# Kernel tuning notes

Measured on AMD Instinct MI355X. Metric: run time of the kernel, lower is better.

## Reference

```python
import jax, jax.numpy as jnp
import numpy as np

B, S, D, H, PF = 2, 2048, 1024, 16, 4096
HD = D // H
EPS = 1e-5


def _rope_tables(seq_len, dim, theta=10000.0):
    freqs = 1.0 / (theta ** (np.arange(0, dim, 2)[: dim // 2].astype(np.float32) / dim))
    ang = np.outer(np.arange(seq_len, dtype=np.float32), freqs)  # [S, D/2]
    return jnp.asarray(np.cos(ang)), jnp.asarray(np.sin(ang))


def setup_inputs() -> dict:
    key = jax.random.key(0)
    ks = jax.random.split(key, 16)
    s = 0.02
    inp = {
        "src": jax.random.normal(ks[0], (B, S, D), dtype=jnp.float32),
        "Wq": jax.random.normal(ks[1], (D, D), dtype=jnp.float32) * s,
        "bq": jnp.zeros((D,), jnp.float32),
        "Wk": jax.random.normal(ks[2], (D, D), dtype=jnp.float32) * s,
        "bk": jnp.zeros((D,), jnp.float32),
        "Wv": jax.random.normal(ks[3], (D, D), dtype=jnp.float32) * s,
        "bv": jnp.zeros((D,), jnp.float32),
        "Wo": jax.random.normal(ks[4], (D, D), dtype=jnp.float32) * s,
        "bo": jnp.zeros((D,), jnp.float32),
        "ln1_g": jnp.ones((D,), jnp.float32),
        "ln1_b": jnp.zeros((D,), jnp.float32),
        "W1": jax.random.normal(ks[5], (D, PF), dtype=jnp.float32) * s,
        "b1": jnp.zeros((PF,), jnp.float32),
        "W2": jax.random.normal(ks[6], (PF, D), dtype=jnp.float32) * s,
        "b2": jnp.zeros((D,), jnp.float32),
        "ln2_g": jnp.ones((D,), jnp.float32),
        "ln2_b": jnp.zeros((D,), jnp.float32),
    }
    cos, sin = _rope_tables(S, D)
    inp["rope_cos"] = cos
    inp["rope_sin"] = sin
    return inp


def _apply_rope(x, cos, sin):
    # x: [B, S, D]; rotate adjacent channel pairs as complex numbers (Meta LLaMA style)
    xp = x.reshape(x.shape[0], x.shape[1], -1, 2)
    a, b = xp[..., 0], xp[..., 1]
    c = cos[None, : x.shape[1]]
    s = sin[None, : x.shape[1]]
    out = jnp.stack([a * c - b * s, a * s + b * c], axis=-1)
    return out.reshape(x.shape)


def _layer_norm(x, g, b):
    mu = x.mean(-1, keepdims=True)
    var = ((x - mu) ** 2).mean(-1, keepdims=True)
    return (x - mu) * jax.lax.rsqrt(var + EPS) * g + b


def reference(src, Wq, bq, Wk, bk, Wv, bv, Wo, bo, ln1_g, ln1_b,
              W1, b1, W2, b2, ln2_g, ln2_b, rope_cos, rope_sin):
    bsz, seq, _ = src.shape
    Q = src @ Wq + bq
    K = src @ Wk + bk
    V = src @ Wv + bv
    Q = _apply_rope(Q, rope_cos, rope_sin)
    K = _apply_rope(K, rope_cos, rope_sin)
    # split heads: [B, H, S, HD]
    Q = Q.reshape(bsz, seq, H, HD).transpose(0, 2, 1, 3)
    K = K.reshape(bsz, seq, H, HD).transpose(0, 2, 1, 3)
    V = V.reshape(bsz, seq, H, HD).transpose(0, 2, 1, 3)
    scale = 1.0 / jnp.sqrt(jnp.float32(HD))
    energy = jnp.einsum("bhqd,bhkd->bhqk", Q, K) * scale
    attn = jax.nn.softmax(energy, axis=-1)
    x = jnp.einsum("bhqk,bhkd->bhqd", attn, V)
    x = x.transpose(0, 2, 1, 3).reshape(bsz, seq, D)
    attn_out = x @ Wo + bo
    # residual + LayerNorm
    h = _layer_norm(src + attn_out, ln1_g, ln1_b)
    # positionwise feedforward
    ff = jax.nn.relu(h @ W1 + b1) @ W2 + b2
    return _layer_norm(h + ff, ln2_g, ln2_b)
```

## Files before the change

### kernel.cpp

```cpp
#include <hip/hip_runtime.h>

#define SEQ 2048
#define DIM 1024
#define NH 16
#define HDIM 64
#define PFF 4096
#define NROWS 4096
#define BATCH 2
#define NQKV 3072

typedef unsigned short u16;
typedef unsigned int u32;
typedef __attribute__((ext_vector_type(8))) short short8;
typedef __attribute__((ext_vector_type(4))) float f32x4;
typedef __attribute__((ext_vector_type(16))) float f32x16;

__device__ inline float b2f(u16 u){ return __uint_as_float(((u32)u)<<16); }
__device__ inline u16 f2b(float f){
  u32 u = __float_as_uint(f);
  u32 r = u + 0x7FFFu + ((u>>16)&1u);
  return (u16)(r>>16);
}
__device__ __forceinline__ float fexp2(float x){
  float r; asm("v_exp_f32 %0, %1" : "=v"(r) : "v"(x)); return r;
}
__device__ __forceinline__ float fmax3(float a, float b, float c){
  float r; asm("v_max3_f32 %0, %1, %2, %3" : "=v"(r) : "v"(a), "v"(b), "v"(c)); return r;
}

#define AS1C(p) ((const __attribute__((address_space(1))) unsigned int*)(p))
#define AS3P(p) ((__attribute__((address_space(3))) unsigned int*)(p))

__global__ void k_cast_bf16(const float* __restrict__ in, u16* __restrict__ out, int n4){
  int i = blockIdx.x*256 + threadIdx.x;
  if (i >= n4) return;
  float4 v = ((const float4*)in)[i];
  ushort4 o;
  o.x = f2b(v.x); o.y = f2b(v.y); o.z = f2b(v.z); o.w = f2b(v.w);
  ((ushort4*)out)[i] = o;
}

__global__ __launch_bounds__(256) void k_transpose_cast(const float* __restrict__ in,
                                                        u16* __restrict__ out, int R, int C){
  __shared__ float tile[32][33];
  int tx = threadIdx.x & 31, ty = threadIdx.x >> 5;
  int c0 = blockIdx.x*32, r0 = blockIdx.y*32;
  #pragma unroll
  for (int i=0;i<4;++i)
    tile[ty+i*8][tx] = in[(size_t)(r0+ty+i*8)*C + c0 + tx];
  __syncthreads();
  #pragma unroll
  for (int i=0;i<4;++i)
    out[(size_t)(c0+ty+i*8)*R + r0 + tx] = f2b(tile[tx][ty+i*8]);
}

__global__ __launch_bounds__(256) void k_transpose_v(const u16* __restrict__ QKV, u16* __restrict__ VT){
  __shared__ u16 tile[32][34];
  int tx = threadIdx.x & 31, ty = threadIdx.x >> 5;
  int d0 = blockIdx.x*32, r0 = blockIdx.y*32;
  #pragma unroll
  for (int i=0;i<4;++i)
    tile[ty+i*8][tx] = QKV[(size_t)(r0+ty+i*8)*NQKV + 2048 + d0 + tx];
  __syncthreads();
  #pragma unroll
  for (int i=0;i<4;++i)
    VT[(size_t)(d0+ty+i*8)*NROWS + r0 + tx] = tile[tx][ty+i*8];
}

__global__ void k_pack3(const float* __restrict__ a, const float* __restrict__ b,
                        const float* __restrict__ c, float* __restrict__ o){
  int i = blockIdx.x*256 + threadIdx.x;
  if (i >= NQKV) return;
  o[i] = i < 1024 ? a[i] : (i < 2048 ? b[i-1024] : c[i-2048]);
}

template<bool RELU, bool BF16OUT, int SPLIT>
__global__ __launch_bounds__(512, 2) void k_gemm256(
    const u16* __restrict__ A, const u16* __restrict__ Bt,
    const float* __restrict__ bias, void* __restrict__ Cp,
    int M, int N, int Kc, int lda, int ldb){
  extern __shared__ char lds[];
  const int tid = threadIdx.x;
  const int lane = tid & 63, wid = tid >> 6;
  const int quad = lane >> 4, l15 = lane & 15;
  const int wm = wid >> 2, wn = wid & 3;
  const int ro = (l15*4 + quad)*16;
  const int srow = lane >> 2;
  const int sk   = (lane & 3)*8;
  const int nwg = gridDim.x * gridDim.y;
  int lid = blockIdx.y * gridDim.x + blockIdx.x;
  lid = (lid & 7) * (nwg >> 3) + (lid >> 3);
  const int bx = lid % gridDim.x, by = lid / gridDim.x;
  const int rowBase = by*256, colBase = bx*256;
  const u16* Az = A  + (size_t)blockIdx.z * Kc;
  const u16* Bz = Bt + (size_t)blockIdx.z * Kc;

  f32x4 acc[8][4] = {};

  auto stage2 = [&](int buf, int k0, int i){
    int idx = i*8 + wid;
    int rs = idx >> 1, ks = idx & 1;
    const u16* ga = Az + (size_t)(rowBase + rs*16 + srow)*lda + k0 + ks*32 + sk;
    __builtin_amdgcn_global_load_lds(AS1C(ga), AS3P(lds + buf*65536 + idx*1024), 16, 0, 0);
    const u16* gb = Bz + (size_t)(colBase + rs*16 + srow)*ldb + k0 + ks*32 + sk;
    __builtin_amdgcn_global_load_lds(AS1C(gb), AS3P(lds + buf*65536 + 32768 + idx*1024), 16, 0, 0);
  };

  #pragma unroll
  for (int i=0;i<4;++i) stage2(0, 0, i);
  __syncthreads();

  const int NT = Kc >> 6;
  #pragma unroll 1
  for (int t=0; t<NT; ++t){
    const int buf = t & 1;
    const bool pf = (t+1 < NT);
    const int k0n = (t+1)*64;
    char* Ab = lds + buf*65536;
    char* Bb = Ab + 32768;
    short8 a0[4][2], a1[4][2], b0[2][2], b1[2][2];

    #pragma unroll
    for (int mf=0; mf<4; ++mf)
      #pragma unroll
      for (int kk=0; kk<2; ++kk)
        a0[mf][kk] = *(const short8*)(Ab + ((wm*8+mf)*2+kk)*1024 + ro);
    #pragma unroll
    for (int nf=0; nf<2; ++nf)
      #pragma unroll
      for (int kk=0; kk<2; ++kk)
        b0[nf][kk] = *(const short8*)(Bb + ((wn*4+nf)*2+kk)*1024 + ro);
    if (pf){ stage2(buf^1, k0n, 0); stage2(buf^1, k0n, 1); }
    __builtin_amdgcn_s_barrier();
    __builtin_amdgcn_s_setprio(1);
    #pragma unroll
    for (int mf=0; mf<4; ++mf)
      #pragma unroll
      for (int nf=0; nf<2; ++nf)
        #pragma unroll
        for (int kk=0; kk<2; ++kk)
          acc[mf][nf] = __builtin_amdgcn_mfma_f32_16x16x32_bf16(a0[mf][kk], b0[nf][kk], acc[mf][nf], 0,0,0);
    __builtin_amdgcn_s_setprio(0);
    __builtin_amdgcn_s_barrier();

    #pragma unroll
    for (int nf=0; nf<2; ++nf)
      #pragma unroll
      for (int kk=0; kk<2; ++kk)
        b1[nf][kk] = *(const short8*)(Bb + ((wn*4+2+nf)*2+kk)*1024 + ro);
    if (pf){ stage2(buf^1, k0n, 2); stage2(buf^1, k0n, 3); }
    __builtin_amdgcn_s_barrier();
    __builtin_amdgcn_s_setprio(1);
    #pragma unroll
    for (int mf=0; mf<4; ++mf)
      #pragma unroll
      for (int nf=0; nf<2; ++nf)
        #pragma unroll
        for (int kk=0; kk<2; ++kk)
          acc[mf][2+nf] = __builtin_amdgcn_mfma_f32_16x16x32_bf16(a0[mf][kk], b1[nf][kk], acc[mf][2+nf], 0,0,0);
    __builtin_amdgcn_s_setprio(0);
    __builtin_amdgcn_s_barrier();

    #pragma unroll
    for (int mf=0; mf<4; ++mf)
      #pragma unroll
      for (int kk=0; kk<2; ++kk)
        a1[mf][kk] = *(const short8*)(Ab + ((wm*8+4+mf)*2+kk)*1024 + ro);
    __builtin_amdgcn_s_barrier();
    __builtin_amdgcn_s_setprio(1);
    #pragma unroll
    for (int mf=0; mf<4; ++mf)
      #pragma unroll
      for (int nf=0; nf<2; ++nf)
        #pragma unroll
        for (int kk=0; kk<2; ++kk)
          acc[4+mf][2+nf] = __builtin_amdgcn_mfma_f32_16x16x32_bf16(a1[mf][kk], b1[nf][kk], acc[4+mf][2+nf], 0,0,0);
    __builtin_amdgcn_s_setprio(0);
    __builtin_amdgcn_s_barrier();

    if (pf) asm volatile("s_waitcnt vmcnt(0)" ::: "memory");
    __builtin_amdgcn_s_barrier();
    __builtin_amdgcn_s_setprio(1);
    #pragma unroll
    for (int mf=0; mf<4; ++mf)
      #pragma unroll
      for (int nf=0; nf<2; ++nf)
        #pragma unroll
        for (int kk=0; kk<2; ++kk)
          acc[4+mf][nf] = __builtin_amdgcn_mfma_f32_16x16x32_bf16(a1[mf][kk], b0[nf][kk], acc[4+mf][nf], 0,0,0);
    __builtin_amdgcn_s_setprio(0);
    __builtin_amdgcn_s_barrier();
  }

  u16* Cb = (u16*)Cp + (SPLIT > 1 ? (size_t)blockIdx.z * M * N : 0);
  float* Cf = (float*)Cp + (SPLIT > 1 ? (size_t)blockIdx.z * M * N : 0);
  #pragma unroll
  for (int mf=0; mf<8; ++mf){
    #pragma unroll
    for (int nf=0; nf<4; ++nf){
      int col = colBase + wn*64 + nf*16 + l15;
      float bv = (SPLIT == 1 || blockIdx.z == 0) ? bias[col] : 0.f;
      #pragma unroll
      for (int j=0; j<4; ++j){
        int row = rowBase + wm*128 + mf*16 + quad*4 + j;
        float v = acc[mf][nf][j] + bv;
        if (RELU) v = fmaxf(v, 0.f);
        if (BF16OUT) Cb[(size_t)row*N + col] = f2b(v);
        else         Cf[(size_t)row*N + col] = v;
      }
    }
  }
}

template<bool RELU, bool BF16OUT, bool BIAS>
__global__ __launch_bounds__(256) void k_gemm(
    const u16* __restrict__ A, const u16* __restrict__ Bt,
    const float* __restrict__ bias, void* __restrict__ Cp,
    int M, int N, int Kc, int lda, int ldb){
  __shared__ __align__(16) char lds[32768];
  const int tid = threadIdx.x;
  const int lane = tid & 63, wid = tid >> 6;
  const int quad = lane >> 4, l15 = lane & 15;
  const int wr = wid >> 1, wc = wid & 1;
  const int nwg = gridDim.x * gridDim.y;
  int lid = blockIdx.y * gridDim.x + blockIdx.x;
  lid = (lid & 7) * (nwg >> 3) + (lid >> 3);
  const int bx = lid % gridDim.x, by = lid / gridDim.x;
  const int rowBase = by * 128, colBase = bx * 128;
  const u16* Az = A  + (size_t)blockIdx.z * Kc;
  const u16* Bz = Bt + (size_t)blockIdx.z * Kc;
  f32x4 acc[4][4] = {};
  const int srow = lane >> 3;
  const int scol = lane & 7;
  for (int k0 = 0; k0 < Kc; k0 += 64) {
    __syncthreads();
    #pragma unroll
    for (int i=0;i<4;++i){
      int wch = wid*4 + i;
      int row = wch*8 + srow;
      int c   = scol ^ (row & 7);
      const u16* ga = Az + (size_t)(rowBase+row)*lda + k0 + c*8;
      __builtin_amdgcn_global_load_lds(AS1C(ga), AS3P(lds + wch*1024), 16, 0, 0);
      const u16* gb = Bz + (size_t)(colBase+row)*ldb + k0 + c*8;
      __builtin_amdgcn_global_load_lds(AS1C(gb), AS3P(lds + 16384 + wch*1024), 16, 0, 0);
    }
    __syncthreads();
    #pragma unroll
    for (int kk=0;kk<2;++kk){
      short8 af[4], bfr[4];
      #pragma unroll
      for (int m=0;m<4;++m){
        int r = wr*64 + m*16 + l15;
        af[m] = *(const short8*)(lds + ((r*128 + kk*64 + quad*16) ^ ((r&7)<<4)));
      }
      #pragma unroll
      for (int n=0;n<4;++n){
        int r = wc*64 + n*16 + l15;
        bfr[n] = *(const short8*)(lds + 16384 + ((r*128 + kk*64 + quad*16) ^ ((r&7)<<4)));
      }
      __builtin_amdgcn_s_setprio(1);
      #pragma unroll
      for (int m=0;m<4;++m)
        #pragma unroll
        for (int n=0;n<4;++n)
          acc[m][n] = __builtin_amdgcn_mfma_f32_16x16x32_bf16(af[m], bfr[n], acc[m][n], 0,0,0);
      __builtin_amdgcn_s_setprio(0);
    }
  }
  float* Cf = (float*)Cp + (size_t)blockIdx.z * M * N;
  #pragma unroll
  for (int m=0;m<4;++m){
    #pragma unroll
    for (int n=0;n<4;++n){
      int col = colBase + wc*64 + n*16 + l15;
      float bv = (BIAS && blockIdx.z == 0) ? bias[col] : 0.f;
      #pragma unroll
      for (int j=0;j<4;++j){
        int row = rowBase + wr*64 + m*16 + quad*4 + j;
        float v = acc[m][n][j] + bv;
        if (RELU) v = fmaxf(v, 0.f);
        if (BF16OUT) ((u16*)Cp)[(size_t)row*N + col] = f2b(v);
        else         Cf[(size_t)row*N + col] = v;
      }
    }
  }
}

__global__ void k_rope(u16* __restrict__ QKV,
                       const float* __restrict__ cosT, const float* __restrict__ sinT){
  int idx = blockIdx.x*256 + threadIdx.x;
  int row = idx >> 9, p = idx & 511;
  int s = row & (SEQ-1);
  float c = cosT[s*512 + p], sn = sinT[s*512 + p];
  u16* qp = QKV + (size_t)row*NQKV + 2*p;
  u16* kp = qp + 1024;
  ushort2 q = *(ushort2*)qp;
  ushort2 k = *(ushort2*)kp;
  float qx = b2f(q.x), qy = b2f(q.y), kx = b2f(k.x), ky = b2f(k.y);
  const float scale = 0.125f * 1.44269504f;
  ushort2 qo, ko;
  qo.x = f2b((qx*c - qy*sn)*scale);
  qo.y = f2b((qx*sn + qy*c)*scale);
  ko.x = f2b(kx*c - ky*sn);
  ko.y = f2b(kx*sn + ky*c);
  *(ushort2*)qp = qo;
  *(ushort2*)kp = ko;
}

__global__ __launch_bounds__(256) void k_attn(
    const u16* __restrict__ QKV, const u16* __restrict__ VT, u16* __restrict__ Xo){
  const int qt = blockIdx.x, h = blockIdx.y, b = blockIdx.z;
  const int tid = threadIdx.x, lane = tid & 63, wid = tid >> 6;
  const int l31 = lane & 31, hi = lane >> 5;
  __shared__ __align__(16) char lds[32768];
  const int srow = lane >> 3, scol = lane & 7;

  short8 qf[4];
  {
    const u16* qrow = QKV + (size_t)(b*SEQ + qt*128 + wid*32 + l31)*NQKV + h*HDIM;
    #pragma unroll
    for (int dk=0; dk<4; ++dk)
      qf[dk] = *(const short8*)(qrow + dk*16 + 8*hi);
  }
  float m_run = -1e30f, s_run = 0.f;
  f32x16 oacc[2] = {};
  const size_t krow0 = (size_t)(b*SEQ);

  auto do_stage = [&](int buf, int kt){
    char* kdst = lds + buf*16384;
    char* vdst = kdst + 8192;
    #pragma unroll
    for (int i=0;i<2;++i){
      int wch = wid*2 + i;
      int row = wch*8 + srow;
      int c = scol ^ (row & 7);
      const u16* gk = QKV + (krow0 + kt*64 + row)*NQKV + 1024 + h*HDIM + c*8;
      __builtin_amdgcn_global_load_lds(AS1C(gk), AS3P(kdst + wch*1024), 16, 0, 0);
      const u16* gv = VT + (size_t)(h*HDIM + row)*NROWS + b*SEQ + kt*64 + c*8;
      __builtin_amdgcn_global_load_lds(AS1C(gv), AS3P(vdst + wch*1024), 16, 0, 0);
    }
  };

  auto do_tile = [&](int buf){
    char* kb = lds + buf*16384;
    char* vb = kb + 8192;
    f32x16 pacc[2] = {};
    __builtin_amdgcn_s_setprio(1);
    #pragma unroll
    for (int kbk=0;kbk<2;++kbk){
      #pragma unroll
      for (int dk=0;dk<4;++dk){
        int row = kbk*32 + l31;
        short8 kf = *(const short8*)(kb + ((row*128 + dk*32 + 16*hi) ^ ((row&7)<<4)));
        pacc[kbk] = __builtin_amdgcn_mfma_f32_32x32x16_bf16(kf, qf[dk], pacc[kbk], 0,0,0);
      }
    }
    __builtin_amdgcn_s_setprio(0);
    float tmax = fmaxf(pacc[0][0], pacc[0][1]);
    #pragma unroll
    for (int r=2;r<16;r+=2) tmax = fmax3(tmax, pacc[0][r], pacc[0][r+1]);
    #pragma unroll
    for (int r=0;r<16;r+=2) tmax = fmax3(tmax, pacc[1][r], pacc[1][r+1]);
    tmax = fmaxf(tmax, __shfl_xor(tmax, 32));
    if (__any(tmax > m_run + 8.0f)){
      float mnew = fmaxf(m_run, tmax);
      float a = fexp2(m_run - mnew);
      s_run *= a;
      m_run = mnew;
      #pragma unroll
      for (int r=0;r<16;++r){
        int src = (r&3) + 8*(r>>2) + 4*hi;
        float ar = __shfl(a, src);
        oacc[0][r] *= ar;
        oacc[1][r] *= ar;
      }
    }
    float p[2][16];
    float psum = 0.f;
    #pragma unroll
    for (int kbk=0;kbk<2;++kbk)
      #pragma unroll
      for (int r=0;r<16;++r){
        float e = fexp2(pacc[kbk][r] - m_run);
        p[kbk][r] = e;
        psum += e;
      }
    psum += __shfl_xor(psum, 32);
    s_run += psum;
    short8 pa[4];
    #pragma unroll
    for (int kbk=0;kbk<2;++kbk){
      #pragma unroll
      for (int s=0;s<2;++s){
        u32 X0, X1, Y0, Y1;
        asm("v_cvt_pk_bf16_f32 %0, %1, %2" : "=v"(X0) : "v"(p[kbk][8*s+0]), "v"(p[kbk][8*s+1]));
        asm("v_cvt_pk_bf16_f32 %0, %1, %2" : "=v"(X1) : "v"(p[kbk][8*s+2]), "v"(p[kbk][8*s+3]));
        asm("v_cvt_pk_bf16_f32 %0, %1, %2" : "=v"(Y0) : "v"(p[kbk][8*s+4]), "v"(p[kbk][8*s+5]));
        asm("v_cvt_pk_bf16_f32 %0, %1, %2" : "=v"(Y1) : "v"(p[kbk][8*s+6]), "v"(p[kbk][8*s+7]));
        asm volatile("v_permlane32_swap_b32 %0, %1" : "+v"(X0), "+v"(Y0));
        asm volatile("v_permlane32_swap_b32 %0, %1" : "+v"(X1), "+v"(Y1));
        union { u32 w[4]; short8 s8; } pu;
        pu.w[0] = X0; pu.w[1] = X1; pu.w[2] = Y0; pu.w[3] = Y1;
        pa[2*kbk+s] = pu.s8;
      }
    }
    __builtin_amdgcn_s_setprio(1);
    #pragma unroll
    for (int db=0;db<2;++db){
      #pragma unroll
      for (int ks=0;ks<4;++ks){
        int row = db*32 + l31;
        short8 vf = *(const short8*)(vb + ((row*128 + ks*32 + 16*hi) ^ ((row&7)<<4)));
        oacc[db] = __builtin_amdgcn_mfma_f32_32x32x16_bf16(pa[ks], vf, oacc[db], 0,0,0);
      }
    }
    __builtin_amdgcn_s_setprio(0);
  };

  do_stage(0, 0);
  __syncthreads();
  const int NT = SEQ/64;
  #pragma unroll 1
  for (int kt=0; kt<NT; kt+=2){
    do_stage(1, kt+1);
    do_tile(0);
    __syncthreads();
    if (kt+2 < NT) do_stage(0, kt+2);
    do_tile(1);
    __syncthreads();
  }
  #pragma unroll
  for (int r=0;r<16;++r){
    int crow = (r&3) + 8*(r>>2) + 4*hi;
    float sq = __shfl(s_run, crow);
    float rs = __builtin_amdgcn_rcpf(sq);
    int grow = b*SEQ + qt*128 + wid*32 + crow;
    Xo[(size_t)grow*DIM + h*HDIM + l31]      = f2b(oacc[0][r] * rs);
    Xo[(size_t)grow*DIM + h*HDIM + 32 + l31] = f2b(oacc[1][r] * rs);
  }
}

template<int PARTS, bool WBF>
__global__ __launch_bounds__(256) void k_ln(
    const float* __restrict__ a, const float* __restrict__ p0, const float* __restrict__ p1,
    const float* __restrict__ g, const float* __restrict__ be,
    float* __restrict__ outf, u16* __restrict__ outb){
  const int row = blockIdx.x, tid = threadIdx.x;
  __shared__ float red[8];
  float4 av = ((const float4*)(a  + (size_t)row*DIM))[tid];
  float4 b0 = ((const float4*)(p0 + (size_t)row*DIM))[tid];
  float4 b1 = ((const float4*)(p1 + (size_t)row*DIM))[tid];
  float x0 = av.x+b0.x+b1.x, x1 = av.y+b0.y+b1.y, x2 = av.z+b0.z+b1.z, x3 = av.w+b0.w+b1.w;
  float s = x0+x1+x2+x3;
  #pragma unroll
  for (int o=32;o>=1;o>>=1) s += __shfl_down(s, o);
  if ((tid&63)==0) red[tid>>6] = s;
  __syncthreads();
  float mean = (red[0]+red[1]+red[2]+red[3]) * (1.0f/DIM);
  float d0=x0-mean, d1=x1-mean, d2=x2-mean, d3=x3-mean;
  float vs = d0*d0+d1*d1+d2*d2+d3*d3;
  #pragma unroll
  for (int o=32;o>=1;o>>=1) vs += __shfl_down(vs, o);
  if ((tid&63)==0) red[4+(tid>>6)] = vs;
  __syncthreads();
  float var = (red[4]+red[5]+red[6]+red[7]) * (1.0f/DIM);
  float rs = rsqrtf(var + 1e-5f);
  float4 gv = ((const float4*)g)[tid];
  float4 bev = ((const float4*)be)[tid];
  float4 y;
  y.x = d0*rs*gv.x + bev.x;
  y.y = d1*rs*gv.y + bev.y;
  y.z = d2*rs*gv.z + bev.z;
  y.w = d3*rs*gv.w + bev.w;
  ((float4*)(outf + (size_t)row*DIM))[tid] = y;
  if (WBF){
    ushort4 o4; o4.x=f2b(y.x); o4.y=f2b(y.y); o4.z=f2b(y.z); o4.w=f2b(y.w);
    ((ushort4*)(outb + (size_t)row*DIM))[tid] = o4;
  }
}

template<int PARTS>
__global__ __launch_bounds__(256) void k_lnp(
    const float* __restrict__ a, const u16* __restrict__ p,
    const float* __restrict__ g, const float* __restrict__ be,
    float* __restrict__ outf){
  const int row = blockIdx.x, tid = threadIdx.x;
  __shared__ float red[8];
  float4 av = ((const float4*)(a + (size_t)row*DIM))[tid];
  float x0 = av.x, x1 = av.y, x2 = av.z, x3 = av.w;
  #pragma unroll
  for (int z=0; z<PARTS; ++z){
    ushort4 pv = ((const ushort4*)(p + (size_t)z*NROWS*DIM + (size_t)row*DIM))[tid];
    x0 += b2f(pv.x); x1 += b2f(pv.y); x2 += b2f(pv.z); x3 += b2f(pv.w);
  }
  float s = x0+x1+x2+x3;
  #pragma unroll
  for (int o=32;o>=1;o>>=1) s += __shfl_down(s, o);
  if ((tid&63)==0) red[tid>>6] = s;
  __syncthreads();
  float mean = (red[0]+red[1]+red[2]+red[3]) * (1.0f/DIM);
  float d0=x0-mean, d1=x1-mean, d2=x2-mean, d3=x3-mean;
  float vs = d0*d0+d1*d1+d2*d2+d3*d3;
  #pragma unroll
  for (int o=32;o>=1;o>>=1) vs += __shfl_down(vs, o);
  if ((tid&63)==0) red[4+(tid>>6)] = vs;
  __syncthreads();
  float var = (red[4]+red[5]+red[6]+red[7]) * (1.0f/DIM);
  float rs = rsqrtf(var + 1e-5f);
  float4 gv = ((const float4*)g)[tid];
  float4 bev = ((const float4*)be)[tid];
  float4 y;
  y.x = d0*rs*gv.x + bev.x;
  y.y = d1*rs*gv.y + bev.y;
  y.z = d2*rs*gv.z + bev.z;
  y.w = d3*rs*gv.w + bev.w;
  ((float4*)(outf + (size_t)row*DIM))[tid] = y;
}

extern "C" void kernel_launch(void* const* d_in, const int* in_sizes, int n_in,
                              void* d_out, int out_size, void* d_ws, size_t ws_size,
                              hipStream_t stream){
  (void)in_sizes; (void)n_in; (void)out_size; (void)ws_size;
  const float* src  = (const float*)d_in[0];
  const float* Wq   = (const float*)d_in[1];
  const float* bq   = (const float*)d_in[2];
  const float* Wk   = (const float*)d_in[3];
  const float* bk   = (const float*)d_in[4];
  const float* Wv   = (const float*)d_in[5];
  const float* bv   = (const float*)d_in[6];
  const float* Wo   = (const float*)d_in[7];
  const float* bo   = (const float*)d_in[8];
  const float* ln1g = (const float*)d_in[9];
  const float* ln1b = (const float*)d_in[10];
  const float* W1   = (const float*)d_in[11];
  const float* b1   = (const float*)d_in[12];
  const float* W2   = (const float*)d_in[13];
  const float* b2   = (const float*)d_in[14];
  const float* ln2g = (const float*)d_in[15];
  const float* ln2b = (const float*)d_in[16];
  const float* rc   = (const float*)d_in[17];
  const float* rsn  = (const float*)d_in[18];

  char* ws = (char*)d_ws;
  const size_t MB = (size_t)1<<20;
  u16* Xbf   = (u16*)(ws);
  u16* QKV   = (u16*)(ws + 8*MB);
  u16* VTb   = (u16*)(ws + 32*MB);
  float* aop   = (float*)(ws + 8*MB);
  u16* ff2b  = (u16*)(ws + 8*MB);
  u16* xat   = (u16*)(ws + 40*MB);
  u16* hbf   = (u16*)(ws + 48*MB);
  u16* WqkvT = (u16*)(ws + 56*MB);
  u16* WoT   = (u16*)(ws + 62*MB);
  u16* W1T   = (u16*)(ws + 64*MB);
  u16* W2T   = (u16*)(ws + 72*MB);
  u16* ff1   = (u16*)(ws + 80*MB);
  float* h   = (float*)(ws + 112*MB);
  float* bqkv= (float*)(ws + 128*MB);
  const size_t P16 = 16*MB/4;

  hipFuncSetAttribute((const void*)&k_gemm256<false,true,1>,
                      hipFuncAttributeMaxDynamicSharedMemorySize, 131072);
  hipFuncSetAttribute((const void*)&k_gemm256<true,true,1>,
                      hipFuncAttributeMaxDynamicSharedMemorySize, 131072);
  hipFuncSetAttribute((const void*)&k_gemm256<false,true,4>,
                      hipFuncAttributeMaxDynamicSharedMemorySize, 131072);

  dim3 blk(256);
  k_cast_bf16<<<dim3(NROWS*DIM/1024), blk, 0, stream>>>(src, Xbf, NROWS*DIM/4);
  k_transpose_cast<<<dim3(DIM/32, DIM/32), blk, 0, stream>>>(Wq, WqkvT, DIM, DIM);
  k_transpose_cast<<<dim3(DIM/32, DIM/32), blk, 0, stream>>>(Wk, WqkvT + (size_t)1024*1024, DIM, DIM);
  k_transpose_cast<<<dim3(DIM/32, DIM/32), blk, 0, stream>>>(Wv, WqkvT + (size_t)2048*1024, DIM, DIM);
  k_transpose_cast<<<dim3(DIM/32, DIM/32), blk, 0, stream>>>(Wo, WoT, DIM, DIM);
  k_transpose_cast<<<dim3(PFF/32, DIM/32), blk, 0, stream>>>(W1, W1T, DIM, PFF);
  k_transpose_cast<<<dim3(DIM/32, PFF/32), blk, 0, stream>>>(W2, W2T, PFF, DIM);
  k_pack3<<<dim3(12), blk, 0, stream>>>(bq, bk, bv, bqkv);

  k_gemm256<false,true,1><<<dim3(NQKV/256, NROWS/256), dim3(512), 131072, stream>>>(
      Xbf, WqkvT, bqkv, QKV, NROWS, NQKV, DIM, DIM, DIM);
  k_rope<<<dim3(NROWS*512/256), blk, 0, stream>>>(QKV, rc, rsn);
  k_transpose_v<<<dim3(DIM/32, NROWS/32), blk, 0, stream>>>(QKV, VTb);
  k_attn<<<dim3(SEQ/128, NH, BATCH), blk, 0, stream>>>(QKV, VTb, xat);
  k_gemm<false,false,true><<<dim3(DIM/128, NROWS/128, 2), blk, 0, stream>>>(
      xat, WoT, bo, aop, NROWS, DIM, 512, DIM, DIM);
  k_ln<2,true><<<dim3(NROWS), blk, 0, stream>>>(src, aop, aop + P16, ln1g, ln1b, h, hbf);
  k_gemm256<true,true,1><<<dim3(PFF/256, NROWS/256), dim3(512), 131072, stream>>>(
      hbf, W1T, b1, ff1, NROWS, PFF, DIM, DIM, DIM);
  k_gemm256<false,true,4><<<dim3(DIM/256, NROWS/256, 4), dim3(512), 131072, stream>>>(
      ff1, W2T, b2, ff2b, NROWS, DIM, 1024, PFF, PFF);
  k_lnp<4><<<dim3(NROWS), blk, 0, stream>>>(h, ff2b, ln2g, ln2b, (float*)d_out);
}
```

Before: 250.8 us.

## Triple-buffer attention KV tiles and overlap QK with softmax-PV; bf16 out-proj partials

Result: no change. 254.9 us (+1.6%).

```diff
diff --git a/kernel.cpp b/kernel.cpp
--- a/kernel.cpp
+++ b/kernel.cpp
@@ -267,6 +267,7 @@
       __builtin_amdgcn_s_setprio(0);
     }
   }
+  u16* Cb = (u16*)Cp + (size_t)blockIdx.z * M * N;
   float* Cf = (float*)Cp + (size_t)blockIdx.z * M * N;
   #pragma unroll
   for (int m=0;m<4;++m){
@@ -279,7 +280,7 @@
         int row = rowBase + wr*64 + m*16 + quad*4 + j;
         float v = acc[m][n][j] + bv;
         if (RELU) v = fmaxf(v, 0.f);
-        if (BF16OUT) ((u16*)Cp)[(size_t)row*N + col] = f2b(v);
+        if (BF16OUT) Cb[(size_t)row*N + col] = f2b(v);
         else         Cf[(size_t)row*N + col] = v;
       }
     }
@@ -312,7 +313,7 @@
   const int qt = blockIdx.x, h = blockIdx.y, b = blockIdx.z;
   const int tid = threadIdx.x, lane = tid & 63, wid = tid >> 6;
   const int l31 = lane & 31, hi = lane >> 5;
-  __shared__ __align__(16) char lds[32768];
+  __shared__ __align__(16) char lds[49152];
   const int srow = lane >> 3, scol = lane & 7;
 
   short8 qf[4];
@@ -326,8 +327,8 @@
   f32x16 oacc[2] = {};
   const size_t krow0 = (size_t)(b*SEQ);
 
-  auto do_stage = [&](int buf, int kt){
-    char* kdst = lds + buf*16384;
+  auto stage = [&](int kt){
+    char* kdst = lds + (kt%3)*16384;
     char* vdst = kdst + 8192;
     #pragma unroll
     for (int i=0;i<2;++i){
@@ -341,10 +342,10 @@
     }
   };
 
-  auto do_tile = [&](int buf){
-    char* kb = lds + buf*16384;
-    char* vb = kb + 8192;
-    f32x16 pacc[2] = {};
+  auto qk = [&](int kt, f32x16 (&pacc)[2]){
+    char* kb = lds + (kt%3)*16384;
+    #pragma unroll
+    for (int r=0;r<16;++r){ pacc[0][r]=0.f; pacc[1][r]=0.f; }
     __builtin_amdgcn_s_setprio(1);
     #pragma unroll
     for (int kbk=0;kbk<2;++kbk){
@@ -356,6 +357,10 @@
       }
     }
     __builtin_amdgcn_s_setprio(0);
+  };
+
+  auto sm_pv = [&](int kt, f32x16 (&pacc)[2]){
+    char* vb = lds + (kt%3)*16384 + 8192;
     float tmax = fmaxf(pacc[0][0], pacc[0][1]);
     #pragma unroll
     for (int r=2;r<16;r+=2) tmax = fmax3(tmax, pacc[0][r], pacc[0][r+1]);
@@ -375,28 +380,26 @@
         oacc[1][r] *= ar;
       }
     }
-    float p[2][16];
     float psum = 0.f;
-    #pragma unroll
-    for (int kbk=0;kbk<2;++kbk)
-      #pragma unroll
-      for (int r=0;r<16;++r){
-        float e = fexp2(pacc[kbk][r] - m_run);
-        p[kbk][r] = e;
-        psum += e;
-      }
-    psum += __shfl_xor(psum, 32);
-    s_run += psum;
     short8 pa[4];
     #pragma unroll
     for (int kbk=0;kbk<2;++kbk){
       #pragma unroll
       for (int s=0;s<2;++s){
+        float e0 = fexp2(pacc[kbk][8*s+0] - m_run);
+        float e1 = fexp2(pacc[kbk][8*s+1] - m_run);
+        float e2 = fexp2(pacc[kbk][8*s+2] - m_run);
+        float e3 = fexp2(pacc[kbk][8*s+3] - m_run);
+        float e4 = fexp2(pacc[kbk][8*s+4] - m_run);
+        float e5 = fexp2(pacc[kbk][8*s+5] - m_run);
+        float e6 = fexp2(pacc[kbk][8*s+6] - m_run);
+        float e7 = fexp2(pacc[kbk][8*s+7] - m_run);
+        psum += (e0+e1)+(e2+e3)+((e4+e5)+(e6+e7));
         u32 X0, X1, Y0, Y1;
-        asm("v_cvt_pk_bf16_f32 %0, %1, %2" : "=v"(X0) : "v"(p[kbk][8*s+0]), "v"(p[kbk][8*s+1]));
-        asm("v_cvt_pk_bf16_f32 %0, %1, %2" : "=v"(X1) : "v"(p[kbk][8*s+2]), "v"(p[kbk][8*s+3]));
-        asm("v_cvt_pk_bf16_f32 %0, %1, %2" : "=v"(Y0) : "v"(p[kbk][8*s+4]), "v"(p[kbk][8*s+5]));
-        asm("v_cvt_pk_bf16_f32 %0, %1, %2" : "=v"(Y1) : "v"(p[kbk][8*s+6]), "v"(p[kbk][8*s+7]));
+        asm("v_cvt_pk_bf16_f32 %0, %1, %2" : "=v"(X0) : "v"(e0), "v"(e1));
+        asm("v_cvt_pk_bf16_f32 %0, %1, %2" : "=v"(X1) : "v"(e2), "v"(e3));
+        asm("v_cvt_pk_bf16_f32 %0, %1, %2" : "=v"(Y0) : "v"(e4), "v"(e5));
+        asm("v_cvt_pk_bf16_f32 %0, %1, %2" : "=v"(Y1) : "v"(e6), "v"(e7));
         asm volatile("v_permlane32_swap_b32 %0, %1" : "+v"(X0), "+v"(Y0));
         asm volatile("v_permlane32_swap_b32 %0, %1" : "+v"(X1), "+v"(Y1));
         union { u32 w[4]; short8 s8; } pu;
@@ -404,6 +407,8 @@
         pa[2*kbk+s] = pu.s8;
       }
     }
+    psum += __shfl_xor(psum, 32);
+    s_run += psum;
     __builtin_amdgcn_s_setprio(1);
     #pragma unroll
     for (int db=0;db<2;++db){
@@ -417,17 +422,35 @@
     __builtin_amdgcn_s_setprio(0);
   };
 
-  do_stage(0, 0);
-  __syncthreads();
+  f32x16 paccA[2], paccB[2];
   const int NT = SEQ/64;
+  stage(0);
+  stage(1);
+  asm volatile("s_waitcnt vmcnt(4)" ::: "memory");
+  __builtin_amdgcn_s_barrier();
+  qk(0, paccA);
   #pragma unroll 1
-  for (int kt=0; kt<NT; kt+=2){
-    do_stage(1, kt+1);
-    do_tile(0);
-    __syncthreads();
-    if (kt+2 < NT) do_stage(0, kt+2);
-    do_tile(1);
-    __syncthreads();
+  for (int t=0; t<NT; t+=2){
+    if (t+2 < NT){
+      stage(t+2);
+      asm volatile("s_waitcnt vmcnt(4)" ::: "memory");
+    } else {
+      asm volatile("s_waitcnt vmcnt(0)" ::: "memory");
+    }
+    __builtin_amdgcn_s_barrier();
+    qk(t+1, paccB);
+    sm_pv(t, paccA);
+    __builtin_amdgcn_s_barrier();
+    if (t+3 < NT){
+      stage(t+3);
+      asm volatile("s_waitcnt vmcnt(4)" ::: "memory");
+    } else {
+      asm volatile("s_waitcnt vmcnt(0)" ::: "memory");
+    }
+    __builtin_amdgcn_s_barrier();
+    if (t+2 < NT) qk(t+2, paccA);
+    sm_pv(t+1, paccB);
+    __builtin_amdgcn_s_barrier();
   }
   #pragma unroll
   for (int r=0;r<16;++r){
@@ -441,16 +464,19 @@
 }
 
 template<int PARTS, bool WBF>
-__global__ __launch_bounds__(256) void k_ln(
-    const float* __restrict__ a, const float* __restrict__ p0, const float* __restrict__ p1,
+__global__ __launch_bounds__(256) void k_lnp(
+    const float* __restrict__ a, const u16* __restrict__ p,
     const float* __restrict__ g, const float* __restrict__ be,
     float* __restrict__ outf, u16* __restrict__ outb){
   const int row = blockIdx.x, tid = threadIdx.x;
   __shared__ float red[8];
-  float4 av = ((const float4*)(a  + (size_t)row*DIM))[tid];
-  float4 b0 = ((const float4*)(p0 + (size_t)row*DIM))[tid];
-  float4 b1 = ((const float4*)(p1 + (size_t)row*DIM))[tid];
-  float x0 = av.x+b0.x+b1.x, x1 = av.y+b0.y+b1.y, x2 = av.z+b0.z+b1.z, x3 = av.w+b0.w+b1.w;
+  float4 av = ((const float4*)(a + (size_t)row*DIM))[tid];
+  float x0 = av.x, x1 = av.y, x2 = av.z, x3 = av.w;
+  #pragma unroll
+  for (int z=0; z<PARTS; ++z){
+    ushort4 pv = ((const ushort4*)(p + (size_t)z*NROWS*DIM + (size_t)row*DIM))[tid];
+    x0 += b2f(pv.x); x1 += b2f(pv.y); x2 += b2f(pv.z); x3 += b2f(pv.w);
+  }
   float s = x0+x1+x2+x3;
   #pragma unroll
   for (int o=32;o>=1;o>>=1) s += __shfl_down(s, o);
@@ -477,44 +503,6 @@
     ushort4 o4; o4.x=f2b(y.x); o4.y=f2b(y.y); o4.z=f2b(y.z); o4.w=f2b(y.w);
     ((ushort4*)(outb + (size_t)row*DIM))[tid] = o4;
   }
-}
-
-template<int PARTS>
-__global__ __launch_bounds__(256) void k_lnp(
-    const float* __restrict__ a, const u16* __restrict__ p,
-    const float* __restrict__ g, const float* __restrict__ be,
-    float* __restrict__ outf){
-  const int row = blockIdx.x, tid = threadIdx.x;
-  __shared__ float red[8];
-  float4 av = ((const float4*)(a + (size_t)row*DIM))[tid];
-  float x0 = av.x, x1 = av.y, x2 = av.z, x3 = av.w;
-  #pragma unroll
-  for (int z=0; z<PARTS; ++z){
-    ushort4 pv = ((const ushort4*)(p + (size_t)z*NROWS*DIM + (size_t)row*DIM))[tid];
-    x0 += b2f(pv.x); x1 += b2f(pv.y); x2 += b2f(pv.z); x3 += b2f(pv.w);
-  }
-  float s = x0+x1+x2+x3;
-  #pragma unroll
-  for (int o=32;o>=1;o>>=1) s += __shfl_down(s, o);
-  if ((tid&63)==0) red[tid>>6] = s;
-  __syncthreads();
-  float mean = (red[0]+red[1]+red[2]+red[3]) * (1.0f/DIM);
-  float d0=x0-mean, d1=x1-mean, d2=x2-mean, d3=x3-mean;
-  float vs = d0*d0+d1*d1+d2*d2+d3*d3;
-  #pragma unroll
-  for (int o=32;o>=1;o>>=1) vs += __shfl_down(vs, o);
-  if ((tid&63)==0) red[4+(tid>>6)] = vs;
-  __syncthreads();
-  float var = (red[4]+red[5]+red[6]+red[7]) * (1.0f/DIM);
-  float rs = rsqrtf(var + 1e-5f);
-  float4 gv = ((const float4*)g)[tid];
-  float4 bev = ((const float4*)be)[tid];
-  float4 y;
-  y.x = d0*rs*gv.x + bev.x;
-  y.y = d1*rs*gv.y + bev.y;
-  y.z = d2*rs*gv.z + bev.z;
-  y.w = d3*rs*gv.w + bev.w;
-  ((float4*)(outf + (size_t)row*DIM))[tid] = y;
 }
 
 extern "C" void kernel_launch(void* const* d_in, const int* in_sizes, int n_in,
@@ -546,7 +534,7 @@
   u16* Xbf   = (u16*)(ws);
   u16* QKV   = (u16*)(ws + 8*MB);
   u16* VTb   = (u16*)(ws + 32*MB);
-  float* aop   = (float*)(ws + 8*MB);
+  u16* aob   = (u16*)(ws + 8*MB);
   u16* ff2b  = (u16*)(ws + 8*MB);
   u16* xat   = (u16*)(ws + 40*MB);
   u16* hbf   = (u16*)(ws + 48*MB);
@@ -557,7 +545,6 @@
   u16* ff1   = (u16*)(ws + 80*MB);
   float* h   = (float*)(ws + 112*MB);
   float* bqkv= (float*)(ws + 128*MB);
-  const size_t P16 = 16*MB/4;
 
   hipFuncSetAttribute((const void*)&k_gemm256<false,true,1>,
                       hipFuncAttributeMaxDynamicSharedMemorySize, 131072);
@@ -581,12 +568,12 @@
   k_rope<<<dim3(NROWS*512/256), blk, 0, stream>>>(QKV, rc, rsn);
   k_transpose_v<<<dim3(DIM/32, NROWS/32), blk, 0, stream>>>(QKV, VTb);
   k_attn<<<dim3(SEQ/128, NH, BATCH), blk, 0, stream>>>(QKV, VTb, xat);
-  k_gemm<false,false,true><<<dim3(DIM/128, NROWS/128, 2), blk, 0, stream>>>(
-      xat, WoT, bo, aop, NROWS, DIM, 512, DIM, DIM);
-  k_ln<2,true><<<dim3(NROWS), blk, 0, stream>>>(src, aop, aop + P16, ln1g, ln1b, h, hbf);
+  k_gemm<false,true,true><<<dim3(DIM/128, NROWS/128, 2), blk, 0, stream>>>(
+      xat, WoT, bo, aob, NROWS, DIM, 512, DIM, DIM);
+  k_lnp<2,true><<<dim3(NROWS), blk, 0, stream>>>(src, aob, ln1g, ln1b, h, hbf);
   k_gemm256<true,true,1><<<dim3(PFF/256, NROWS/256), dim3(512), 131072, stream>>>(
       hbf, W1T, b1, ff1, NROWS, PFF, DIM, DIM, DIM);
   k_gemm256<false,true,4><<<dim3(DIM/256, NROWS/256, 4), dim3(512), 131072, stream>>>(
       ff1, W2T, b2, ff2b, NROWS, DIM, 1024, PFF, PFF);
-  k_lnp<4><<<dim3(NROWS), blk, 0, stream>>>(h, ff2b, ln2g, ln2b, (float*)d_out);
-}
+  k_lnp<4,false><<<dim3(NROWS), blk, 0, stream>>>(h, ff2b, ln2g, ln2b, (float*)d_out, nullptr);
+}
```

## Use bf16 split-K partials for Wo GEMM, drop fp32 h, merge weight transposes

Applied to the files above, without the earlier changes.

Result: no change. 247.9 us (-1.2%).

```diff
diff --git a/kernel.cpp b/kernel.cpp
--- a/kernel.cpp
+++ b/kernel.cpp
@@ -52,6 +52,25 @@
   #pragma unroll
   for (int i=0;i<4;++i)
     out[(size_t)(c0+ty+i*8)*R + r0 + tx] = f2b(tile[tx][ty+i*8]);
+}
+
+__global__ __launch_bounds__(256) void k_transpose_cast4(
+    const float* __restrict__ w0, const float* __restrict__ w1,
+    const float* __restrict__ w2, const float* __restrict__ w3,
+    u16* __restrict__ o012, u16* __restrict__ o3){
+  __shared__ float tile[32][33];
+  const int z = blockIdx.z;
+  const float* in = z==0 ? w0 : (z==1 ? w1 : (z==2 ? w2 : w3));
+  u16* out = (z<3) ? (o012 + (size_t)z*DIM*DIM) : o3;
+  int tx = threadIdx.x & 31, ty = threadIdx.x >> 5;
+  int c0 = blockIdx.x*32, r0 = blockIdx.y*32;
+  #pragma unroll
+  for (int i=0;i<4;++i)
+    tile[ty+i*8][tx] = in[(size_t)(r0+ty+i*8)*DIM + c0 + tx];
+  __syncthreads();
+  #pragma unroll
+  for (int i=0;i<4;++i)
+    out[(size_t)(c0+ty+i*8)*DIM + r0 + tx] = f2b(tile[tx][ty+i*8]);
 }
 
 __global__ __launch_bounds__(256) void k_transpose_v(const u16* __restrict__ QKV, u16* __restrict__ VT){
@@ -212,80 +231,6 @@
   }
 }
 
-template<bool RELU, bool BF16OUT, bool BIAS>
-__global__ __launch_bounds__(256) void k_gemm(
-    const u16* __restrict__ A, const u16* __restrict__ Bt,
-    const float* __restrict__ bias, void* __restrict__ Cp,
-    int M, int N, int Kc, int lda, int ldb){
-  __shared__ __align__(16) char lds[32768];
-  const int tid = threadIdx.x;
-  const int lane = tid & 63, wid = tid >> 6;
-  const int quad = lane >> 4, l15 = lane & 15;
-  const int wr = wid >> 1, wc = wid & 1;
-  const int nwg = gridDim.x * gridDim.y;
-  int lid = blockIdx.y * gridDim.x + blockIdx.x;
-  lid = (lid & 7) * (nwg >> 3) + (lid >> 3);
-  const int bx = lid % gridDim.x, by = lid / gridDim.x;
-  const int rowBase = by * 128, colBase = bx * 128;
-  const u16* Az = A  + (size_t)blockIdx.z * Kc;
-  const u16* Bz = Bt + (size_t)blockIdx.z * Kc;
-  f32x4 acc[4][4] = {};
-  const int srow = lane >> 3;
-  const int scol = lane & 7;
-  for (int k0 = 0; k0 < Kc; k0 += 64) {
-    __syncthreads();
-    #pragma unroll
-    for (int i=0;i<4;++i){
-      int wch = wid*4 + i;
-      int row = wch*8 + srow;
-      int c   = scol ^ (row & 7);
-      const u16* ga = Az + (size_t)(rowBase+row)*lda + k0 + c*8;
-      __builtin_amdgcn_global_load_lds(AS1C(ga), AS3P(lds + wch*1024), 16, 0, 0);
-      const u16* gb = Bz + (size_t)(colBase+row)*ldb + k0 + c*8;
-      __builtin_amdgcn_global_load_lds(AS1C(gb), AS3P(lds + 16384 + wch*1024), 16, 0, 0);
-    }
-    __syncthreads();
-    #pragma unroll
-    for (int kk=0;kk<2;++kk){
-      short8 af[4], bfr[4];
-      #pragma unroll
-      for (int m=0;m<4;++m){
-        int r = wr*64 + m*16 + l15;
-        af[m] = *(const short8*)(lds + ((r*128 + kk*64 + quad*16) ^ ((r&7)<<4)));
-      }
-      #pragma unroll
-      for (int n=0;n<4;++n){
-        int r = wc*64 + n*16 + l15;
-        bfr[n] = *(const short8*)(lds + 16384 + ((r*128 + kk*64 + quad*16) ^ ((r&7)<<4)));
-      }
-      __builtin_amdgcn_s_setprio(1);
-      #pragma unroll
-      for (int m=0;m<4;++m)
-        #pragma unroll
-        for (int n=0;n<4;++n)
-          acc[m][n] = __builtin_amdgcn_mfma_f32_16x16x32_bf16(af[m], bfr[n], acc[m][n], 0,0,0);
-      __builtin_amdgcn_s_setprio(0);
-    }
-  }
-  float* Cf = (float*)Cp + (size_t)blockIdx.z * M * N;
-  #pragma unroll
-  for (int m=0;m<4;++m){
-    #pragma unroll
-    for (int n=0;n<4;++n){
-      int col = colBase + wc*64 + n*16 + l15;
-      float bv = (BIAS && blockIdx.z == 0) ? bias[col] : 0.f;
-      #pragma unroll
-      for (int j=0;j<4;++j){
-        int row = rowBase + wr*64 + m*16 + quad*4 + j;
-        float v = acc[m][n][j] + bv;
-        if (RELU) v = fmaxf(v, 0.f);
-        if (BF16OUT) ((u16*)Cp)[(size_t)row*N + col] = f2b(v);
-        else         Cf[(size_t)row*N + col] = v;
-      }
-    }
-  }
-}
-
 __global__ void k_rope(u16* __restrict__ QKV,
                        const float* __restrict__ cosT, const float* __restrict__ sinT){
   int idx = blockIdx.x*256 + threadIdx.x;
@@ -440,17 +385,26 @@
   }
 }
 
-template<int PARTS, bool WBF>
-__global__ __launch_bounds__(256) void k_ln(
-    const float* __restrict__ a, const float* __restrict__ p0, const float* __restrict__ p1,
+template<int PARTS, bool WF32, bool WBF, bool RESBF>
+__global__ __launch_bounds__(256) void k_lnp(
+    const void* __restrict__ a, const u16* __restrict__ p,
     const float* __restrict__ g, const float* __restrict__ be,
     float* __restrict__ outf, u16* __restrict__ outb){
   const int row = blockIdx.x, tid = threadIdx.x;
   __shared__ float red[8];
-  float4 av = ((const float4*)(a  + (size_t)row*DIM))[tid];
-  float4 b0 = ((const float4*)(p0 + (size_t)row*DIM))[tid];
-  float4 b1 = ((const float4*)(p1 + (size_t)row*DIM))[tid];
-  float x0 = av.x+b0.x+b1.x, x1 = av.y+b0.y+b1.y, x2 = av.z+b0.z+b1.z, x3 = av.w+b0.w+b1.w;
+  float x0, x1, x2, x3;
+  if (RESBF){
+    ushort4 av = ((const ushort4*)((const u16*)a + (size_t)row*DIM))[tid];
+    x0 = b2f(av.x); x1 = b2f(av.y); x2 = b2f(av.z); x3 = b2f(av.w);
+  } else {
+    float4 av = ((const float4*)((const float*)a + (size_t)row*DIM))[tid];
+    x0 = av.x; x1 = av.y; x2 = av.z; x3 = av.w;
+  }
+  #pragma unroll
+  for (int z=0; z<PARTS; ++z){
+    ushort4 pv = ((const ushort4*)(p + (size_t)z*NROWS*DIM + (size_t)row*DIM))[tid];
+    x0 += b2f(pv.x); x1 += b2f(pv.y); x2 += b2f(pv.z); x3 += b2f(pv.w);
+  }
   float s = x0+x1+x2+x3;
   #pragma unroll
   for (int o=32;o>=1;o>>=1) s += __shfl_down(s, o);
@@ -472,49 +426,12 @@
   y.y = d1*rs*gv.y + bev.y;
   y.z = d2*rs*gv.z + bev.z;
   y.w = d3*rs*gv.w + bev.w;
-  ((float4*)(outf + (size_t)row*DIM))[tid] = y;
+  if (WF32)
+    ((float4*)(outf + (size_t)row*DIM))[tid] = y;
   if (WBF){
     ushort4 o4; o4.x=f2b(y.x); o4.y=f2b(y.y); o4.z=f2b(y.z); o4.w=f2b(y.w);
     ((ushort4*)(outb + (size_t)row*DIM))[tid] = o4;
   }
-}
-
-template<int PARTS>
-__global__ __launch_bounds__(256) void k_lnp(
-    const float* __restrict__ a, const u16* __restrict__ p,
-    const float* __restrict__ g, const float* __restrict__ be,
-    float* __restrict__ outf){
-  const int row = blockIdx.x, tid = threadIdx.x;
-  __shared__ float red[8];
-  float4 av = ((const float4*)(a + (size_t)row*DIM))[tid];
-  float x0 = av.x, x1 = av.y, x2 = av.z, x3 = av.w;
-  #pragma unroll
-  for (int z=0; z<PARTS; ++z){
-    ushort4 pv = ((const ushort4*)(p + (size_t)z*NROWS*DIM + (size_t)row*DIM))[tid];
-    x0 += b2f(pv.x); x1 += b2f(pv.y); x2 += b2f(pv.z); x3 += b2f(pv.w);
-  }
-  float s = x0+x1+x2+x3;
-  #pragma unroll
-  for (int o=32;o>=1;o>>=1) s += __shfl_down(s, o);
-  if ((tid&63)==0) red[tid>>6] = s;
-  __syncthreads();
-  float mean = (red[0]+red[1]+red[2]+red[3]) * (1.0f/DIM);
-  float d0=x0-mean, d1=x1-mean, d2=x2-mean, d3=x3-mean;
-  float vs = d0*d0+d1*d1+d2*d2+d3*d3;
-  #pragma unroll
-  for (int o=32;o>=1;o>>=1) vs += __shfl_down(vs, o);
-  if ((tid&63)==0) red[4+(tid>>6)] = vs;
-  __syncthreads();
-  float var = (red[4]+red[5]+red[6]+red[7]) * (1.0f/DIM);
-  float rs = rsqrtf(var + 1e-5f);
-  float4 gv = ((const float4*)g)[tid];
-  float4 bev = ((const float4*)be)[tid];
-  float4 y;
-  y.x = d0*rs*gv.x + bev.x;
-  y.y = d1*rs*gv.y + bev.y;
-  y.z = d2*rs*gv.z + bev.z;
-  y.w = d3*rs*gv.w + bev.w;
-  ((float4*)(outf + (size_t)row*DIM))[tid] = y;
 }
 
 extern "C" void kernel_launch(void* const* d_in, const int* in_sizes, int n_in,
@@ -546,7 +463,7 @@
   u16* Xbf   = (u16*)(ws);
   u16* QKV   = (u16*)(ws + 8*MB);
   u16* VTb   = (u16*)(ws + 32*MB);
-  float* aop   = (float*)(ws + 8*MB);
+  u16* aob   = (u16*)(ws + 8*MB);
   u16* ff2b  = (u16*)(ws + 8*MB);
   u16* xat   = (u16*)(ws + 40*MB);
   u16* hbf   = (u16*)(ws + 48*MB);
@@ -555,9 +472,7 @@
   u16* W1T   = (u16*)(ws + 64*MB);
   u16* W2T   = (u16*)(ws + 72*MB);
   u16* ff1   = (u16*)(ws + 80*MB);
-  float* h   = (float*)(ws + 112*MB);
   float* bqkv= (float*)(ws + 128*MB);
-  const size_t P16 = 16*MB/4;
 
   hipFuncSetAttribute((const void*)&k_gemm256<false,true,1>,
                       hipFuncAttributeMaxDynamicSharedMemorySize, 131072);
@@ -568,10 +483,7 @@
 
   dim3 blk(256);
   k_cast_bf16<<<dim3(NROWS*DIM/1024), blk, 0, stream>>>(src, Xbf, NROWS*DIM/4);
-  k_transpose_cast<<<dim3(DIM/32, DIM/32), blk, 0, stream>>>(Wq, WqkvT, DIM, DIM);
-  k_transpose_cast<<<dim3(DIM/32, DIM/32), blk, 0, stream>>>(Wk, WqkvT + (size_t)1024*1024, DIM, DIM);
-  k_transpose_cast<<<dim3(DIM/32, DIM/32), blk, 0, stream>>>(Wv, WqkvT + (size_t)2048*1024, DIM, DIM);
-  k_transpose_cast<<<dim3(DIM/32, DIM/32), blk, 0, stream>>>(Wo, WoT, DIM, DIM);
+  k_transpose_cast4<<<dim3(DIM/32, DIM/32, 4), blk, 0, stream>>>(Wq, Wk, Wv, Wo, WqkvT, WoT);
   k_transpose_cast<<<dim3(PFF/32, DIM/32), blk, 0, stream>>>(W1, W1T, DIM, PFF);
   k_transpose_cast<<<dim3(DIM/32, PFF/32), blk, 0, stream>>>(W2, W2T, PFF, DIM);
   k_pack3<<<dim3(12), blk, 0, stream>>>(bq, bk, bv, bqkv);
@@ -581,12 +493,14 @@
   k_rope<<<dim3(NROWS*512/256), blk, 0, stream>>>(QKV, rc, rsn);
   k_transpose_v<<<dim3(DIM/32, NROWS/32), blk, 0, stream>>>(QKV, VTb);
   k_attn<<<dim3(SEQ/128, NH, BATCH), blk, 0, stream>>>(QKV, VTb, xat);
-  k_gemm<false,false,true><<<dim3(DIM/128, NROWS/128, 2), blk, 0, stream>>>(
-      xat, WoT, bo, aop, NROWS, DIM, 512, DIM, DIM);
-  k_ln<2,true><<<dim3(NROWS), blk, 0, stream>>>(src, aop, aop + P16, ln1g, ln1b, h, hbf);
+  k_gemm256<false,true,4><<<dim3(DIM/256, NROWS/256, 4), dim3(512), 131072, stream>>>(
+      xat, WoT, bo, aob, NROWS, DIM, 256, DIM, DIM);
+  k_lnp<4,false,true,false><<<dim3(NROWS), blk, 0, stream>>>(
+      src, aob, ln1g, ln1b, nullptr, hbf);
   k_gemm256<true,true,1><<<dim3(PFF/256, NROWS/256), dim3(512), 131072, stream>>>(
       hbf, W1T, b1, ff1, NROWS, PFF, DIM, DIM, DIM);
   k_gemm256<false,true,4><<<dim3(DIM/256, NROWS/256, 4), dim3(512), 131072, stream>>>(
       ff1, W2T, b2, ff2b, NROWS, DIM, 1024, PFF, PFF);
-  k_lnp<4><<<dim3(NROWS), blk, 0, stream>>>(h, ff2b, ln2g, ln2b, (float*)d_out);
-}
+  k_lnp<4,true,false,true><<<dim3(NROWS), blk, 0, stream>>>(
+      hbf, ff2b, ln2g, ln2b, (float*)d_out, nullptr);
+}
```
